# Optimization experiments

Hardware: AMD Instinct MI355X
Metric: run time of the kernel (lower is better)

The kernel has to match this reference:

```python
import jax, jax.numpy as jnp
import numpy as np
import math

N = 32768
C = 128
K = 16
CHUNK = 2048
LN_EPS = float(C)  # original code calls torch.nn.LayerNorm(C, C): second positional arg is eps -> eps = 128.0 (faithful)


def knn_idx(coords):
    """Brute-force KNN on full coords [N,4] (matches knn_points(x_C, x_C, K=16)), chunked over queries."""
    def one_chunk(q):  # q: [CHUNK,4]
        d = jnp.sum((q[:, None, :] - coords[None, :, :]) ** 2, axis=-1)  # [CHUNK,N]
        return jax.lax.top_k(-d, K)[1]  # ascending distance (return_sorted=True)
    qs = coords.reshape(-1, CHUNK, coords.shape[-1])
    return jax.lax.map(one_chunk, qs).reshape(-1, K)  # [N,K]


def layer_norm(x, g, b):
    mu = jnp.mean(x, axis=-1, keepdims=True)
    var = jnp.mean((x - mu) ** 2, axis=-1, keepdims=True)
    return (x - mu) / jnp.sqrt(var + LN_EPS) * g + b


def self_attention(x_f, xyz_enc, new_feature, qw, qb, kw, kb, vw, vb):
    Q = x_f @ qw + qb                              # [N,C]
    nf = new_feature + xyz_enc                     # [N,K,C]
    Kt = nf @ kw + kb                              # [N,K,C]
    scores = jnp.einsum('nkd,nd->nk', Kt, Q) / math.sqrt(C)
    a = jax.nn.softmax(scores, axis=-1)            # [N,K]
    V = nf @ vw + vb                               # [N,K,C]
    return jnp.einsum('nk,nkd->nd', a, V)          # [N,C]


def setup_inputs() -> dict:
    key = jax.random.key(0)
    ks = jax.random.split(key, 22)
    xyz = jax.random.uniform(ks[0], (N, 3), dtype=jnp.float32) * 100.0
    coords = jnp.concatenate([jnp.zeros((N, 1), jnp.float32), xyz], axis=1)  # [N,4] batch col = 0
    feats = jax.random.normal(ks[1], (N, C), dtype=jnp.float32)
    s = 0.02
    def lin(k, din, dout):
        kw, kb = jax.random.split(k)
        return jax.random.normal(kw, (din, dout), jnp.float32) * s, jax.random.normal(kb, (dout,), jnp.float32) * s
    pos_w, pos_b = lin(ks[2], 3, C)
    pos1_w, pos1_b = lin(ks[3], 3, C)
    qw0, qb0 = lin(ks[4], C, C); kw0, kb0 = lin(ks[5], C, C); vw0, vb0 = lin(ks[6], C, C)
    qw1, qb1 = lin(ks[7], C, C); kw1, kb1 = lin(ks[8], C, C); vw1, vb1 = lin(ks[9], C, C)
    lin_w, lin_b = lin(ks[10], C, C)  # MinkowskiConvolution kernel_size=1 == pointwise linear
    return {
        'coords': coords, 'feats': feats,
        'pos_w': pos_w, 'pos_b': pos_b, 'pos1_w': pos1_w, 'pos1_b': pos1_b,
        'qw0': qw0, 'qb0': qb0, 'kw0': kw0, 'kb0': kb0, 'vw0': vw0, 'vb0': vb0,
        'qw1': qw1, 'qb1': qb1, 'kw1': kw1, 'kb1': kb1, 'vw1': vw1, 'vb1': vb1,
        'lin_w': lin_w, 'lin_b': lin_b,
        'g0': jnp.ones((C,), jnp.float32), 'be0': jnp.zeros((C,), jnp.float32),
        'g1': jnp.ones((C,), jnp.float32), 'be1': jnp.zeros((C,), jnp.float32),
    }


def reference(coords, feats, pos_w, pos_b, pos1_w, pos1_b,
              qw0, qb0, kw0, kb0, vw0, vb0,
              qw1, qb1, kw1, kb1, vw1, vb1,
              lin_w, lin_b, g0, be0, g1, be1):
    idx = knn_idx(coords)                           # [N,K]
    xyz = coords[:, 1:]                             # [N,3]
    new_xyz = xyz[:, None, :] - xyz[idx]            # [N,K,3] relative offsets
    # block 1
    xyz_enc = new_xyz @ pos_w + pos_b               # [N,K,C]
    nf = feats[idx]                                 # gather [N,K,C]
    o = self_attention(feats, xyz_enc, nf, qw0, qb0, kw0, kb0, vw0, vb0)
    # block 2: re-gather updated features with same idx
    nf1 = o[idx]
    xyz_enc1 = new_xyz @ pos1_w + pos1_b
    o = self_attention(o, xyz_enc1, nf1, qw1, qb1, kw1, kb1, vw1, vb1)
    # residual + LN, pointwise conv, residual + LN
    h = layer_norm(feats + o, g0, be0)
    h1 = h @ lin_w + lin_b
    return layer_norm(h + h1, g1, be1)
```

## Files before the change

kernel.cpp:

```cpp
#include <hip/hip_runtime.h>
#include <stdint.h>

#define NPT 32768

typedef unsigned int u32;
typedef unsigned short u16;
typedef unsigned long long u64;

typedef short v8s __attribute__((ext_vector_type(8)));
typedef float v4f __attribute__((ext_vector_type(4)));

__device__ __forceinline__ float b2f(u16 u) {
  union { u32 u; float f; } x; x.u = ((u32)u) << 16; return x.f;
}
__device__ __forceinline__ u16 f2b(float f) {
  union { float f; u32 u; } x; x.f = f;
  u32 u = x.u;
  return (u16)((u + 0x7fffu + ((u >> 16) & 1u)) >> 16);
}
__device__ __forceinline__ bool probe_f32(const void* coords) {
  return ((const u16*)coords)[1] == 0;
}
__device__ __forceinline__ float ldany(const void* p, long i, bool f32) {
  return f32 ? ((const float*)p)[i] : b2f(((const u16*)p)[i]);
}
__device__ __forceinline__ float wsum(float v) {
#pragma unroll
  for (int m = 1; m < 64; m <<= 1) v += __shfl_xor(v, m, 64);
  return v;
}
__device__ __forceinline__ u64 sx64(u64 v, int m) {
  int lo = __shfl_xor((int)(u32)v, m, 64);
  int hi = __shfl_xor((int)(u32)(v >> 32), m, 64);
  return ((u64)(u32)hi << 32) | (u32)lo;
}
__device__ __forceinline__ u64 bc64(u64 v, int src) {
  int lo = __shfl((int)(u32)v, src, 64);
  int hi = __shfl((int)(u32)(v >> 32), src, 64);
  return ((u64)(u32)hi << 32) | (u32)lo;
}
__device__ __forceinline__ u64 up64(u64 v) {
  int lo = __shfl_up((int)(u32)v, 1, 64);
  int hi = __shfl_up((int)(u32)(v >> 32), 1, 64);
  return ((u64)(u32)hi << 32) | (u32)lo;
}
__device__ __forceinline__ float dp8(uint4 a, uint4 b) {
  float s = 0.f;
#pragma unroll
  for (int i = 0; i < 4; i++) {
    u32 ua = ((const u32*)&a)[i], ub = ((const u32*)&b)[i];
    s += b2f((u16)(ua & 0xffffu)) * b2f((u16)(ub & 0xffffu));
    s += b2f((u16)(ua >> 16)) * b2f((u16)(ub >> 16));
  }
  return s;
}

#define GC 16
#define GH 6.25f
#define GINV 0.16f
#define NCELL (GC * GC * GC)

__device__ __forceinline__ int cell1d(float v) {
  int c = (int)(v * GINV);
  return c > (GC - 1) ? (GC - 1) : (c < 0 ? 0 : c);
}

__global__ __launch_bounds__(256) void conv_coords_hist(const void* __restrict__ coords,
                                                        float* __restrict__ cx, float* __restrict__ cy,
                                                        float* __restrict__ cz, int* __restrict__ cellStart,
                                                        int* __restrict__ pcell) {
  const bool f32 = probe_f32(coords);
  int i = blockIdx.x * 256 + threadIdx.x;
  float x = ldany(coords, (long)i * 4 + 1, f32);
  float y = ldany(coords, (long)i * 4 + 2, f32);
  float z = ldany(coords, (long)i * 4 + 3, f32);
  cx[i] = x; cy[i] = y; cz[i] = z;
  int c = (cell1d(z) * GC + cell1d(y)) * GC + cell1d(x);
  pcell[i] = c;
  atomicAdd(&cellStart[c + 1], 1);
}

__global__ __launch_bounds__(256) void conv_featsS(const void* __restrict__ coords,
                                                   const void* __restrict__ feats,
                                                   const float4* __restrict__ sortedP,
                                                   u16* __restrict__ featsS) {
  const bool f32 = probe_f32(coords);
  long i = (long)blockIdx.x * 256 + threadIdx.x;
  int s = (int)(i >> 7), c = (int)(i & 127);
  long orig = (long)__float_as_int(sortedP[s].w);
  featsS[i] = f32 ? f2b(((const float*)feats)[orig * 128 + c]) : ((const u16*)feats)[orig * 128 + c];
}

__global__ __launch_bounds__(256) void grid_scan(int* __restrict__ cellStart, int* __restrict__ cellPtr) {
  __shared__ int part[256];
  const int t = threadIdx.x;
  int local[16]; int s = 0;
#pragma unroll
  for (int i = 0; i < 16; i++) { local[i] = cellStart[1 + t * 16 + i]; s += local[i]; }
  part[t] = s;
  __syncthreads();
  for (int off = 1; off < 256; off <<= 1) {
    int v = (t >= off) ? part[t - off] : 0;
    __syncthreads();
    part[t] += v;
    __syncthreads();
  }
  int run = (t == 0) ? 0 : part[t - 1];
#pragma unroll
  for (int i = 0; i < 16; i++) {
    int c = t * 16 + i;
    cellPtr[c] = run;
    run += local[i];
    cellStart[c + 1] = run;
  }
}

__global__ __launch_bounds__(256) void grid_scatter(const float* __restrict__ cx, const float* __restrict__ cy,
                                                    const float* __restrict__ cz, const int* __restrict__ pcell,
                                                    int* __restrict__ cellPtr, float4* __restrict__ sortedP,
                                                    int* __restrict__ rank) {
  int i = blockIdx.x * 256 + threadIdx.x;
  int c = pcell[i];
  int pos = atomicAdd(&cellPtr[c], 1);
  sortedP[pos] = make_float4(cx[i], cy[i], cz[i], __int_as_float(i));
  rank[i] = pos;
}

__global__ __launch_bounds__(256) void knn_grid(const float4* __restrict__ sortedP,
                                                const int* __restrict__ cellStart,
                                                const int* __restrict__ rank,
                                                u16* __restrict__ idxout) {
  const int lane = threadIdx.x & 63;
  const int q = blockIdx.x * 4 + (threadIdx.x >> 6);
  const float4 p = sortedP[q];
  const float qx = p.x, qy = p.y, qz = p.z;
  const int qcx = cell1d(qx), qcy = cell1d(qy), qcz = cell1d(qz);

  u64 R = ~0ull;

  auto key_of = [&](int g) -> u64 {
    float4 sp = sortedP[g];
    float dx = __fsub_rn(qx, sp.x), dy = __fsub_rn(qy, sp.y), dzc = __fsub_rn(qz, sp.z);
    float d = __fadd_rn(__fadd_rn(__fmul_rn(dx, dx), __fmul_rn(dy, dy)), __fmul_rn(dzc, dzc));
    return ((u64)__float_as_uint(d) << 32) | (u32)__float_as_int(sp.w);
  };

  auto insert_one = [&](u64 kk) {
    u64 prev = up64(R);
    if (lane == 0) prev = 0ull;
    R = (kk < R) ? ((kk >= prev) ? kk : prev) : R;
  };

  auto batch_merge = [&](u64 key) {
    u64 k15 = bc64(R, 15);
    u64 mask = __ballot(key < k15);
    if (mask == 0ull) return;
    int pcount = __popcll(mask);
    if (pcount <= 12) {
      while (mask) {
        int s = __ffsll((long long)mask) - 1;
        mask &= mask - 1ull;
        u64 kk = bc64(key, s);
        if (kk < bc64(R, 15)) insert_one(kk);
      }
      return;
    }
#pragma unroll
    for (int k = 2; k <= 64; k <<= 1) {
#pragma unroll
      for (int j = k >> 1; j > 0; j >>= 1) {
        u64 o = sx64(key, j);
        bool up = ((lane & k) == 0);
        bool lower = ((lane & j) == 0);
        u64 mn = key < o ? key : o;
        u64 mx = key < o ? o : key;
        key = (lower == up) ? mn : mx;
      }
    }
    u64 s = sx64(key, 15);
    u64 mn = R < s ? R : s;
#pragma unroll
    for (int j = 8; j > 0; j >>= 1) {
      u64 o = sx64(mn, j);
      bool lower = ((lane & j) == 0);
      u64 lo = mn < o ? mn : o;
      u64 hi = mn < o ? o : mn;
      mn = lower ? lo : hi;
    }
    R = mn;
  };

  auto scan_range_wave = [&](int s0, int s1) {
    for (int base = s0; base < s1; base += 64) {
      int g = base + lane;
      u64 key = (g < s1) ? key_of(g) : ~0ull;
      batch_merge(key);
    }
  };

  {
    const int rord[9] = { 4, 1, 3, 5, 7, 0, 2, 6, 8 };
    int rs[9], rl[9];
#pragma unroll
    for (int s_ = 0; s_ < 9; s_++) {
      int row = rord[s_];
      int dz = row / 3 - 1, dy = row % 3 - 1;
      int z = qcz + dz, y = qcy + dy;
      if (z < 0 || z > GC - 1 || y < 0 || y > GC - 1) { rs[s_] = 0; rl[s_] = 0; }
      else {
        int rb = (z * GC + y) * GC;
        int xlo = qcx - 1 < 0 ? 0 : qcx - 1;
        int xhi = qcx + 1 > GC - 1 ? GC - 1 : qcx + 1;
        int s = cellStart[rb + xlo], e = cellStart[rb + xhi + 1];
        rs[s_] = s; rl[s_] = e - s;
      }
    }
    int cum[10]; cum[0] = 0;
#pragma unroll
    for (int i = 0; i < 9; i++) cum[i + 1] = cum[i] + rl[i];
    int total = cum[9];
    for (int base = 0; base < total; base += 64) {
      int pp = base + lane;
      u64 key = ~0ull;
      if (pp < total) {
        int g = 0;
#pragma unroll
        for (int i = 0; i < 9; i++) {
          if (pp >= cum[i] && pp < cum[i + 1]) g = rs[i] + (pp - cum[i]);
        }
        key = key_of(g);
      }
      batch_merge(key);
    }
  }

  {
    u64 k15 = bc64(R, 15);
    float d15 = __uint_as_float((u32)(k15 >> 32));
    float b1 = GH * 1.0f;
    if (!(d15 < b1 * b1 * 0.998f)) {
      for (int r = 2; r < GC; ++r) {
        int zlo = qcz - r < 0 ? 0 : qcz - r, zhi = qcz + r > GC - 1 ? GC - 1 : qcz + r;
        for (int z = zlo; z <= zhi; ++z) {
          int adz = z - qcz; adz = adz < 0 ? -adz : adz;
          bool ez = (adz == r);
          int ylo = qcy - r < 0 ? 0 : qcy - r, yhi = qcy + r > GC - 1 ? GC - 1 : qcy + r;
          for (int y = ylo; y <= yhi; ++y) {
            int ady = y - qcy; ady = ady < 0 ? -ady : ady;
            bool ey = (ady == r);
            int rb = (z * GC + y) * GC;
            if (ez || ey) {
              int xlo = qcx - r < 0 ? 0 : qcx - r, xhi = qcx + r > GC - 1 ? GC - 1 : qcx + r;
              scan_range_wave(cellStart[rb + xlo], cellStart[rb + xhi + 1]);
            } else {
              int xm = qcx - r, xp = qcx + r;
              if (xm >= 0) scan_range_wave(cellStart[rb + xm], cellStart[rb + xm + 1]);
              if (xp <= GC - 1) scan_range_wave(cellStart[rb + xp], cellStart[rb + xp + 1]);
            }
          }
        }
        k15 = bc64(R, 15);
        d15 = __uint_as_float((u32)(k15 >> 32));
        float bound = GH * (float)r;
        if (d15 < bound * bound * 0.998f) break;
      }
    }
  }

  if (lane < 16) idxout[(size_t)q * 16 + lane] = (u16)rank[(int)(u32)R];
}

__global__ __launch_bounds__(256) void prep_tables(
    const void* coords,
    const void* pw0, const void* pb0, const void* kw0, const void* kb0, const void* vw0, const void* vb0,
    const void* pw1, const void* pb1, const void* kw1, const void* kb1, const void* vw1, const void* vb1,
    float* __restrict__ tbl, int* __restrict__ cellStart) {
  const bool f32 = probe_f32(coords);
  const int tid = blockIdx.x * 256 + threadIdx.x;
  if (tid <= NCELL) cellStart[tid] = 0;
  const int lane = threadIdx.x & 63;
  const int o = blockIdx.x * 4 + (threadIdx.x >> 6);
  const int l = o >> 10;
  const int rem = o & 1023;
  const void* PW = l ? pw1 : pw0;
  const void* PB = l ? pb1 : pb0;
  const void* KW = l ? kw1 : kw0;
  const void* KB = l ? kb1 : kb0;
  const void* VW = l ? vw1 : vw0;
  const void* VB = l ? vb1 : vb0;
  float acc, extra = 0.f;
  if (rem < 768) {
    bool isV = rem >= 384;
    int r2 = isV ? rem - 384 : rem;
    int i = r2 >> 7, c = r2 & 127;
    const void* W = isV ? VW : KW;
    acc = ldany(PW, i * 128 + lane, f32) * ldany(W, (long)lane * 128 + c, f32)
        + ldany(PW, i * 128 + lane + 64, f32) * ldany(W, (long)(lane + 64) * 128 + c, f32);
  } else {
    bool isV = rem >= 896;
    int c = rem & 127;
    const void* W = isV ? VW : KW;
    const void* B = isV ? VB : KB;
    acc = ldany(PB, lane, f32) * ldany(W, (long)lane * 128 + c, f32)
        + ldany(PB, lane + 64, f32) * ldany(W, (long)(lane + 64) * 128 + c, f32);
    extra = ldany(B, c, f32);
  }
  acc = wsum(acc) + extra;
  if (lane == 0) tbl[l * 1024 + rem] = acc;
}

__global__ __launch_bounds__(256) void prep_bfrag_all(const void* __restrict__ coords,
                                                      const void* __restrict__ qw0, const void* __restrict__ kw0,
                                                      const void* __restrict__ vw0, const void* __restrict__ qw1,
                                                      const void* __restrict__ kw1, const void* __restrict__ vw1,
                                                      const void* __restrict__ linw, u16* __restrict__ Bf0,
                                                      u16* __restrict__ Bf1, u16* __restrict__ BfL) {
  const bool f32 = probe_f32(coords);
  int tid = blockIdx.x * 256 + threadIdx.x;
  const void *w0, *w1, *w2; u16* out; int t;
  if (tid < 49152) { t = tid; w0 = qw0; w1 = kw0; w2 = vw0; out = Bf0; }
  else if (tid < 98304) { t = tid - 49152; w0 = qw1; w1 = kw1; w2 = vw1; out = Bf1; }
  else { t = tid - 98304; w0 = linw; w1 = linw; w2 = linw; out = BfL; }
  int j = t & 7, lane = (t >> 3) & 63, kq = (t >> 9) & 3, tile = t >> 11;
  int k = kq * 32 + ((lane >> 4) << 3) + j;
  int col = tile * 16 + (lane & 15);
  const void* w = (col < 128) ? w0 : ((col < 256) ? w1 : w2);
  long off = (long)k * 128 + (col & 127);
  out[t] = f32 ? f2b(((const float*)w)[off]) : ((const u16*)w)[off];
}

__global__ __launch_bounds__(256) void gemm_kernel(const void* __restrict__ coords,
                                                   const u16* __restrict__ A, const u16* __restrict__ Bf,
                                                   const void* __restrict__ bias, u16* __restrict__ Qb,
                                                   u16* __restrict__ KVb, float* __restrict__ outF,
                                                   int mode, int ntiles) {
  const bool f32 = probe_f32(coords);
  const int lane = threadIdx.x & 63;
  const int wave = threadIdx.x >> 6;
  const int r0 = blockIdx.x * 64 + wave * 16;
  const int quad = lane >> 4, lr = lane & 15;
  v8s a[4];
#pragma unroll
  for (int kq = 0; kq < 4; kq++) {
    union { uint4 u; v8s s; } c;
    c.u = *(const uint4*)(A + (size_t)(r0 + lr) * 128 + kq * 32 + quad * 8);
    a[kq] = c.s;
  }
  for (int tile = 0; tile < ntiles; ++tile) {
    v4f acc = { 0.f, 0.f, 0.f, 0.f };
#pragma unroll
    for (int kq = 0; kq < 4; kq++) {
      union { uint4 u; v8s s; } c;
      c.u = *(const uint4*)(Bf + ((size_t)(tile * 4 + kq) * 64 + lane) * 8);
      acc = __builtin_amdgcn_mfma_f32_16x16x32_bf16(a[kq], c.s, acc, 0, 0, 0);
    }
    int col = tile * 16 + lr;
    if (mode == 0) {
      if (col < 128) {
        float bb = ldany(bias, col, f32);
#pragma unroll
        for (int r = 0; r < 4; r++) Qb[(size_t)(r0 + quad * 4 + r) * 128 + col] = f2b(acc[r] + bb);
      } else {
#pragma unroll
        for (int r = 0; r < 4; r++) KVb[(size_t)(r0 + quad * 4 + r) * 256 + (col - 128)] = f2b(acc[r]);
      }
    } else {
      float bb = ldany(bias, col, f32);
#pragma unroll
      for (int r = 0; r < 4; r++) outF[(size_t)(r0 + quad * 4 + r) * 128 + col] = acc[r] + bb;
    }
  }
}

__global__ __launch_bounds__(256) void attn_kernel(const void* __restrict__ coordsRaw,
                                                   const float4* __restrict__ sortedP,
                                                   const u16* __restrict__ idx,
                                                   const u16* __restrict__ Qb, const u16* __restrict__ KVb,
                                                   const float* __restrict__ tbl, const void* __restrict__ feats,
                                                   const void* __restrict__ g, const void* __restrict__ be,
                                                   u16* __restrict__ outB, int mode) {
  const int lane = threadIdx.x & 63;
  const int n = blockIdx.x * 4 + (threadIdx.x >> 6);
  const int c0 = 2 * lane;
  const int k = lane & 15;
  const int quad = lane >> 4;
  const float4 P = sortedP[n];

  u32 qu = *(const u32*)(Qb + (size_t)n * 128 + c0);
  const float q0 = b2f((u16)(qu & 0xffffu)), q1 = b2f((u16)(qu >> 16));
  float p0 = tbl[c0] * q0 + tbl[c0 + 1] * q1;
  float p1 = tbl[128 + c0] * q0 + tbl[128 + c0 + 1] * q1;
  float p2 = tbl[256 + c0] * q0 + tbl[256 + c0 + 1] * q1;
  float p3 = tbl[768 + c0] * q0 + tbl[768 + c0 + 1] * q1;
#pragma unroll
  for (int m = 1; m < 64; m <<= 1) {
    p0 += __shfl_xor(p0, m, 64);
    p1 += __shfl_xor(p1, m, 64);
    p2 += __shfl_xor(p2, m, 64);
    p3 += __shfl_xor(p3, m, 64);
  }

  const int j = idx[(size_t)n * 16 + k];
  const float4 Pj = sortedP[j];
  const float nx = P.x - Pj.x, ny = P.y - Pj.y, nz = P.z - Pj.z;
  const u16* qrow = Qb + (size_t)n * 128 + quad * 32;
  const u16* krow = KVb + (size_t)j * 256 + quad * 32;
  uint4 qa = *(const uint4*)(qrow), qb2 = *(const uint4*)(qrow + 8);
  uint4 qc = *(const uint4*)(qrow + 16), qd = *(const uint4*)(qrow + 24);
  uint4 ka = *(const uint4*)(krow), kb2 = *(const uint4*)(krow + 8);
  uint4 kc = *(const uint4*)(krow + 16), kd = *(const uint4*)(krow + 24);
  float s = dp8(qa, ka) + dp8(qb2, kb2) + dp8(qc, kc) + dp8(qd, kd);
  s += __shfl_xor(s, 16, 64);
  s += __shfl_xor(s, 32, 64);
  float sc = (s + nx * p0 + ny * p1 + nz * p2 + p3) * 0.08838834764831845f;

  float mx = sc;
#pragma unroll
  for (int m = 1; m < 16; m <<= 1) mx = fmaxf(mx, __shfl_xor(mx, m, 64));
  float e = expf(sc - mx);
  float ssum = e;
#pragma unroll
  for (int m = 1; m < 16; m <<= 1) ssum += __shfl_xor(ssum, m, 64);
  const float a = e / ssum;

  float sA = a, wx = a * nx, wy = a * ny, wz = a * nz;
#pragma unroll
  for (int m = 1; m < 16; m <<= 1) {
    sA += __shfl_xor(sA, m, 64);
    wx += __shfl_xor(wx, m, 64);
    wy += __shfl_xor(wy, m, 64);
    wz += __shfl_xor(wz, m, 64);
  }

  const int base = lane & 48;
  float a0 = 0.f, a1 = 0.f;
#pragma unroll
  for (int k2 = 0; k2 < 16; k2++) {
    float ak = __shfl(a, base + k2, 64);
    int jk = __shfl(j, base + k2, 64);
    u32 u = *(const u32*)(KVb + (size_t)jk * 256 + 128 + c0);
    a0 += ak * b2f((u16)(u & 0xffffu));
    a1 += ak * b2f((u16)(u >> 16));
  }
  float o0 = a0 + wx * tbl[384 + c0] + wy * tbl[512 + c0] + wz * tbl[640 + c0] + sA * tbl[896 + c0];
  float o1 = a1 + wx * tbl[384 + c0 + 1] + wy * tbl[512 + c0 + 1] + wz * tbl[640 + c0 + 1] + sA * tbl[896 + c0 + 1];
  if (mode == 1) {
    const bool f32 = probe_f32(coordsRaw);
    long orig = (long)__float_as_int(P.w);
    float x0 = ldany(feats, orig * 128 + c0, f32) + o0;
    float x1 = ldany(feats, orig * 128 + c0 + 1, f32) + o1;
    float mu = wsum(x0 + x1) * (1.f / 128.f);
    float d0 = x0 - mu, d1 = x1 - mu;
    float var = wsum(d0 * d0 + d1 * d1) * (1.f / 128.f);
    float rinv = 1.0f / sqrtf(var + 128.0f);
    o0 = d0 * rinv * ldany(g, c0, f32) + ldany(be, c0, f32);
    o1 = d1 * rinv * ldany(g, c0 + 1, f32) + ldany(be, c0 + 1, f32);
  }
  ((u32*)outB)[(size_t)n * 64 + lane] = (u32)f2b(o0) | ((u32)f2b(o1) << 16);
}

__global__ __launch_bounds__(256) void ln_final(const void* __restrict__ coords,
                                                const float4* __restrict__ sortedP,
                                                const u16* __restrict__ hB, const float* __restrict__ h1F,
                                                const void* __restrict__ g, const void* __restrict__ be,
                                                void* __restrict__ outAny) {
  const bool f32 = probe_f32(coords);
  const int lane = threadIdx.x & 63;
  const int n = blockIdx.x * 4 + (threadIdx.x >> 6);
  const int c0 = 2 * lane;
  u32 u = *(const u32*)(hB + (size_t)n * 128 + c0);
  float2 h1 = *(const float2*)(h1F + (size_t)n * 128 + c0);
  float x0 = b2f((u16)(u & 0xffffu)) + h1.x;
  float x1 = b2f((u16)(u >> 16)) + h1.y;
  float mu = wsum(x0 + x1) * (1.f / 128.f);
  float d0 = x0 - mu, d1 = x1 - mu;
  float var = wsum(d0 * d0 + d1 * d1) * (1.f / 128.f);
  float rinv = 1.0f / sqrtf(var + 128.0f);
  float y0 = d0 * rinv * ldany(g, c0, f32) + ldany(be, c0, f32);
  float y1 = d1 * rinv * ldany(g, c0 + 1, f32) + ldany(be, c0 + 1, f32);
  size_t orig = (size_t)__float_as_int(sortedP[n].w);
  if (f32) {
    *(float2*)((float*)outAny + orig * 128 + c0) = make_float2(y0, y1);
  } else {
    ((u32*)outAny)[orig * 64 + lane] = (u32)f2b(y0) | ((u32)f2b(y1) << 16);
  }
}

extern "C" void kernel_launch(void* const* d_in, const int* in_sizes, int n_in,
                              void* d_out, int out_size, void* d_ws, size_t ws_size,
                              hipStream_t stream) {
  (void)in_sizes; (void)n_in; (void)out_size; (void)ws_size;
  const void* coords = d_in[0];
  const void* feats = d_in[1];
  const void* pos_w = d_in[2];
  const void* pos_b = d_in[3];
  const void* pos1_w = d_in[4];
  const void* pos1_b = d_in[5];
  const void* qw0 = d_in[6];
  const void* qb0 = d_in[7];
  const void* kw0 = d_in[8];
  const void* kb0 = d_in[9];
  const void* vw0 = d_in[10];
  const void* vb0 = d_in[11];
  const void* qw1 = d_in[12];
  const void* qb1 = d_in[13];
  const void* kw1 = d_in[14];
  const void* kb1 = d_in[15];
  const void* vw1 = d_in[16];
  const void* vb1 = d_in[17];
  const void* lin_w = d_in[18];
  const void* lin_b = d_in[19];
  const void* g0 = d_in[20];
  const void* be0 = d_in[21];
  const void* g1 = d_in[22];
  const void* be1 = d_in[23];

  char* w = (char*)d_ws;
  u16* idxp = (u16*)(w + 0);
  float4* sortedP = (float4*)(w + 1048576);
  int* rank = (int*)(w + 1572864);
  float* cx = (float*)(w + 1703936);
  float* cy = (float*)(w + 1835008);
  float* cz = (float*)(w + 1966080);
  float* tbl = (float*)(w + 2097152);
  u16* Bf0 = (u16*)(w + 2105344);
  u16* Bf1 = (u16*)(w + 2203648);
  u16* BfL = (u16*)(w + 2301952);
  u16* featsS = (u16*)(w + 2334720);
  u16* oS = (u16*)(w + 10723328);
  u16* Qb = (u16*)(w + 19111936);
  u16* KVb = (u16*)(w + 27500544);
  int* cellStart = (int*)(w + 19111936);
  int* cellPtr = (int*)(w + 19132416);
  int* pcell = (int*)(w + 19148800);
  float* h1F = (float*)(w + 19111936);

  hipLaunchKernelGGL(prep_tables, dim3(512), dim3(256), 0, stream, coords,
                     pos_w, pos_b, kw0, kb0, vw0, vb0, pos1_w, pos1_b, kw1, kb1, vw1, vb1, tbl, cellStart);
  hipLaunchKernelGGL(conv_coords_hist, dim3(128), dim3(256), 0, stream, coords, cx, cy, cz, cellStart, pcell);
  hipLaunchKernelGGL(prep_bfrag_all, dim3(448), dim3(256), 0, stream, coords,
                     qw0, kw0, vw0, qw1, kw1, vw1, lin_w, Bf0, Bf1, BfL);

  hipLaunchKernelGGL(grid_scan, dim3(1), dim3(256), 0, stream, cellStart, cellPtr);
  hipLaunchKernelGGL(grid_scatter, dim3(128), dim3(256), 0, stream, cx, cy, cz, pcell, cellPtr, sortedP, rank);
  hipLaunchKernelGGL(conv_featsS, dim3(16384), dim3(256), 0, stream, coords, feats, sortedP, featsS);
  hipLaunchKernelGGL(knn_grid, dim3(8192), dim3(256), 0, stream, sortedP, cellStart, rank, idxp);

  hipLaunchKernelGGL(gemm_kernel, dim3(512), dim3(256), 0, stream, coords, featsS, Bf0, qb0, Qb, KVb,
                     (float*)nullptr, 0, 24);
  hipLaunchKernelGGL(attn_kernel, dim3(8192), dim3(256), 0, stream, coords, sortedP, idxp, Qb, KVb, tbl,
                     (const void*)nullptr, (const void*)nullptr, (const void*)nullptr, oS, 0);
  hipLaunchKernelGGL(gemm_kernel, dim3(512), dim3(256), 0, stream, coords, oS, Bf1, qb1, Qb, KVb,
                     (float*)nullptr, 0, 24);
  hipLaunchKernelGGL(attn_kernel, dim3(8192), dim3(256), 0, stream, coords, sortedP, idxp, Qb, KVb, tbl + 1024,
                     feats, g0, be0, oS, 1);
  hipLaunchKernelGGL(gemm_kernel, dim3(512), dim3(256), 0, stream, coords, oS, BfL, lin_b,
                     (u16*)nullptr, (u16*)nullptr, h1F, 1, 8);
  hipLaunchKernelGGL(ln_final, dim3(8192), dim3(256), 0, stream, coords, sortedP, oS, h1F, g1, be1, d_out);
}
```

Baseline: 328.0 us.

## Process four KNN queries per wavefront using 16-lane groups

The grid KNN kernel now gives each query a 16-lane sub-group instead of a full 64-lane wavefront, so 16 queries run per block and the grid shrinks to a quarter. Candidate scanning, bitonic sorting and top-16 merging use 16-wide group shuffles, and the ballot mask is split per group. The aim is to cut lane waste, since a typical neighbourhood of a few hundred points badly fills 64-wide batches. The trade-off is that groups in one wave can follow different search radii and diverge. The switch from incremental inserts to sorting now happens above 8 qualifying candidates instead of 12.

```diff
diff --git a/kernel.cpp b/kernel.cpp
--- a/kernel.cpp
+++ b/kernel.cpp
@@ -28,21 +28,6 @@
 #pragma unroll
   for (int m = 1; m < 64; m <<= 1) v += __shfl_xor(v, m, 64);
   return v;
-}
-__device__ __forceinline__ u64 sx64(u64 v, int m) {
-  int lo = __shfl_xor((int)(u32)v, m, 64);
-  int hi = __shfl_xor((int)(u32)(v >> 32), m, 64);
-  return ((u64)(u32)hi << 32) | (u32)lo;
-}
-__device__ __forceinline__ u64 bc64(u64 v, int src) {
-  int lo = __shfl((int)(u32)v, src, 64);
-  int hi = __shfl((int)(u32)(v >> 32), src, 64);
-  return ((u64)(u32)hi << 32) | (u32)lo;
-}
-__device__ __forceinline__ u64 up64(u64 v) {
-  int lo = __shfl_up((int)(u32)v, 1, 64);
-  int hi = __shfl_up((int)(u32)(v >> 32), 1, 64);
-  return ((u64)(u32)hi << 32) | (u32)lo;
 }
 __device__ __forceinline__ float dp8(uint4 a, uint4 b) {
   float s = 0.f;
@@ -131,7 +116,9 @@
                                                 const int* __restrict__ rank,
                                                 u16* __restrict__ idxout) {
   const int lane = threadIdx.x & 63;
-  const int q = blockIdx.x * 4 + (threadIdx.x >> 6);
+  const int gl = lane & 15;
+  const int grp = lane >> 4;
+  const int q = blockIdx.x * 16 + (threadIdx.x >> 4);
   const float4 p = sortedP[q];
   const float qx = p.x, qy = p.y, qz = p.z;
   const int qcx = cell1d(qx), qcy = cell1d(qy), qcz = cell1d(qz);
@@ -145,44 +132,61 @@
     return ((u64)__float_as_uint(d) << 32) | (u32)__float_as_int(sp.w);
   };
 
+  auto shfl64 = [&](u64 v, int s) -> u64 {
+    int lo = __shfl((int)(u32)v, s, 16);
+    int hi = __shfl((int)(u32)(v >> 32), s, 16);
+    return ((u64)(u32)hi << 32) | (u32)lo;
+  };
+  auto sxg = [&](u64 v, int m) -> u64 {
+    int lo = __shfl_xor((int)(u32)v, m, 64);
+    int hi = __shfl_xor((int)(u32)(v >> 32), m, 64);
+    return ((u64)(u32)hi << 32) | (u32)lo;
+  };
+  auto upg = [&](u64 v) -> u64 {
+    int lo = __shfl_up((int)(u32)v, 1, 16);
+    int hi = __shfl_up((int)(u32)(v >> 32), 1, 16);
+    return ((u64)(u32)hi << 32) | (u32)lo;
+  };
+
   auto insert_one = [&](u64 kk) {
-    u64 prev = up64(R);
-    if (lane == 0) prev = 0ull;
+    u64 prev = upg(R);
+    if (gl == 0) prev = 0ull;
     R = (kk < R) ? ((kk >= prev) ? kk : prev) : R;
   };
 
   auto batch_merge = [&](u64 key) {
-    u64 k15 = bc64(R, 15);
+    u64 k15 = shfl64(R, 15);
     u64 mask = __ballot(key < k15);
-    if (mask == 0ull) return;
-    int pcount = __popcll(mask);
-    if (pcount <= 12) {
-      while (mask) {
-        int s = __ffsll((long long)mask) - 1;
-        mask &= mask - 1ull;
-        u64 kk = bc64(key, s);
-        if (kk < bc64(R, 15)) insert_one(kk);
+    u32 mymask = (u32)((mask >> (grp * 16)) & 0xffffu);
+    if (mymask == 0) return;
+    int pcount = __popc(mymask);
+    if (pcount <= 8) {
+      u32 mm = mymask;
+      while (mm) {
+        int s = __ffs((int)mm) - 1;
+        mm &= mm - 1;
+        insert_one(shfl64(key, s));
       }
       return;
     }
 #pragma unroll
-    for (int k = 2; k <= 64; k <<= 1) {
+    for (int k = 2; k <= 16; k <<= 1) {
 #pragma unroll
       for (int j = k >> 1; j > 0; j >>= 1) {
-        u64 o = sx64(key, j);
-        bool up = ((lane & k) == 0);
-        bool lower = ((lane & j) == 0);
+        u64 o = sxg(key, j);
+        bool up = ((gl & k) == 0);
+        bool lower = ((gl & j) == 0);
         u64 mn = key < o ? key : o;
         u64 mx = key < o ? o : key;
         key = (lower == up) ? mn : mx;
       }
     }
-    u64 s = sx64(key, 15);
+    u64 s = sxg(key, 15);
     u64 mn = R < s ? R : s;
 #pragma unroll
     for (int j = 8; j > 0; j >>= 1) {
-      u64 o = sx64(mn, j);
-      bool lower = ((lane & j) == 0);
+      u64 o = sxg(mn, j);
+      bool lower = ((gl & j) == 0);
       u64 lo = mn < o ? mn : o;
       u64 hi = mn < o ? o : mn;
       mn = lower ? lo : hi;
@@ -190,9 +194,9 @@
     R = mn;
   };
 
-  auto scan_range_wave = [&](int s0, int s1) {
-    for (int base = s0; base < s1; base += 64) {
-      int g = base + lane;
+  auto scan_range_grp = [&](int s0, int s1) {
+    for (int base = s0; base < s1; base += 16) {
+      int g = base + gl;
       u64 key = (g < s1) ? key_of(g) : ~0ull;
       batch_merge(key);
     }
@@ -219,8 +223,8 @@
 #pragma unroll
     for (int i = 0; i < 9; i++) cum[i + 1] = cum[i] + rl[i];
     int total = cum[9];
-    for (int base = 0; base < total; base += 64) {
-      int pp = base + lane;
+    for (int base = 0; base < total; base += 16) {
+      int pp = base + gl;
       u64 key = ~0ull;
       if (pp < total) {
         int g = 0;
@@ -235,7 +239,7 @@
   }
 
   {
-    u64 k15 = bc64(R, 15);
+    u64 k15 = shfl64(R, 15);
     float d15 = __uint_as_float((u32)(k15 >> 32));
     float b1 = GH * 1.0f;
     if (!(d15 < b1 * b1 * 0.998f)) {
@@ -251,15 +255,15 @@
             int rb = (z * GC + y) * GC;
             if (ez || ey) {
               int xlo = qcx - r < 0 ? 0 : qcx - r, xhi = qcx + r > GC - 1 ? GC - 1 : qcx + r;
-              scan_range_wave(cellStart[rb + xlo], cellStart[rb + xhi + 1]);
+              scan_range_grp(cellStart[rb + xlo], cellStart[rb + xhi + 1]);
             } else {
               int xm = qcx - r, xp = qcx + r;
-              if (xm >= 0) scan_range_wave(cellStart[rb + xm], cellStart[rb + xm + 1]);
-              if (xp <= GC - 1) scan_range_wave(cellStart[rb + xp], cellStart[rb + xp + 1]);
+              if (xm >= 0) scan_range_grp(cellStart[rb + xm], cellStart[rb + xm + 1]);
+              if (xp <= GC - 1) scan_range_grp(cellStart[rb + xp], cellStart[rb + xp + 1]);
             }
           }
         }
-        k15 = bc64(R, 15);
+        k15 = shfl64(R, 15);
         d15 = __uint_as_float((u32)(k15 >> 32));
         float bound = GH * (float)r;
         if (d15 < bound * bound * 0.998f) break;
@@ -267,7 +271,7 @@
     }
   }
 
-  if (lane < 16) idxout[(size_t)q * 16 + lane] = (u16)rank[(int)(u32)R];
+  idxout[(size_t)q * 16 + gl] = (u16)rank[(int)(u32)R];
 }
 
 __global__ __launch_bounds__(256) void prep_tables(
@@ -544,7 +548,7 @@
   hipLaunchKernelGGL(grid_scan, dim3(1), dim3(256), 0, stream, cellStart, cellPtr);
   hipLaunchKernelGGL(grid_scatter, dim3(128), dim3(256), 0, stream, cx, cy, cz, pcell, cellPtr, sortedP, rank);
   hipLaunchKernelGGL(conv_featsS, dim3(16384), dim3(256), 0, stream, coords, feats, sortedP, featsS);
-  hipLaunchKernelGGL(knn_grid, dim3(8192), dim3(256), 0, stream, sortedP, cellStart, rank, idxp);
+  hipLaunchKernelGGL(knn_grid, dim3(2048), dim3(256), 0, stream, sortedP, cellStart, rank, idxp);
 
   hipLaunchKernelGGL(gemm_kernel, dim3(512), dim3(256), 0, stream, coords, featsS, Bf0, qb0, Qb, KVb,
                      (float*)nullptr, 0, 24);
```

Result: faster. 319.7 us (-2.5%).
